# Kernel optimization log

Hardware: AMD Instinct MI355X
Metric: run time of the kernel (lower is better)

The kernel has to match this reference:

```python
import jax, jax.numpy as jnp
import numpy as np

GROUPS = 32
EPS = 1e-3  # keras GroupNormalization default epsilon

def group_norm(x, gamma, beta):
    B, H, W, C = x.shape
    g = GROUPS
    xg = x.reshape(B, H, W, g, C // g)
    mean = jnp.mean(xg, axis=(1, 2, 4), keepdims=True)
    var = jnp.var(xg, axis=(1, 2, 4), keepdims=True)
    xn = (xg - mean) * jax.lax.rsqrt(var + EPS)
    xn = xn.reshape(B, H, W, C)
    return xn * gamma + beta

def setup_inputs() -> dict:
    key = jax.random.key(0)
    ks = jax.random.split(key, 8)
    B, H, W, C = 16, 32, 32, 512
    s = C ** -0.5
    return {
        "x": jax.random.normal(ks[0], (B, H, W, C), jnp.float32),
        "gamma": jnp.ones((C,), jnp.float32),
        "beta": jnp.zeros((C,), jnp.float32),
        "wq": jax.random.normal(ks[1], (C, C), jnp.float32) * s,
        "bq": jnp.zeros((C,), jnp.float32),
        "wk": jax.random.normal(ks[2], (C, C), jnp.float32) * s,
        "bk": jnp.zeros((C,), jnp.float32),
        "wv": jax.random.normal(ks[3], (C, C), jnp.float32) * s,
        "bv": jnp.zeros((C,), jnp.float32),
        "wp": jax.random.normal(ks[4], (C, C), jnp.float32) * s,
        "bp": jnp.zeros((C,), jnp.float32),
        "index": 0,
    }

def reference(x, gamma, beta, wq, bq, wk, bk, wv, bv, wp, bp, index):
    B, H, W, C = x.shape
    N = H * W
    residual = x
    xn = group_norm(x, gamma, beta)
    xf = xn.reshape(B, N, C)
    q = xf @ wq + bq
    k = xf @ wk + bk
    v = xf @ wv + bv
    # full self-attention over all H*W positions (single head)
    scores = jnp.einsum('bnc,bmc->bnm', q, k) * (C ** -0.5)  # [B, N, N]
    attn = jax.nn.softmax(scores, axis=-1)
    out = jnp.einsum('bnm,bmc->bnc', attn, v)
    out = out @ wp + bp
    return out.reshape(B, H, W, C) + residual
```

## Files before the change

kernel.cpp:

```cpp
#include <hip/hip_runtime.h>

typedef __bf16 bf16;
typedef __bf16 bf16x8 __attribute__((ext_vector_type(8)));
typedef __bf16 bf16x4 __attribute__((ext_vector_type(4)));
typedef float  f32x4  __attribute__((ext_vector_type(4)));

#define CDIM   512
#define NPOS   1024
#define NBATCH 16
#define MTOT   (NBATCH * NPOS)
#define WELEMS (CDIM * CDIM)

#define OFF_WT  ((size_t)0)
#define OFF_XN  ((size_t)(2 * 1024 * 1024))
#define OFF_Q   (OFF_XN + (size_t)MTOT * CDIM * 2)
#define OFF_K   (OFF_Q  + (size_t)MTOT * CDIM * 2)
#define OFF_VT  (OFF_K  + (size_t)MTOT * CDIM * 2)
#define OFF_S   (OFF_VT + (size_t)MTOT * CDIM * 2)
#define OFF_P   (OFF_S  + (size_t)NBATCH * NPOS * NPOS * 4)
#define OFF_O   OFF_XN

__device__ __forceinline__ void gload16(const bf16* g, bf16* l) {
    __builtin_amdgcn_global_load_lds(
        (const __attribute__((address_space(1))) void*)g,
        (__attribute__((address_space(3))) void*)l, 16, 0, 0);
}

__global__ __launch_bounds__(256) void transpose_cast(
    const float* __restrict__ w0, const float* __restrict__ w1,
    const float* __restrict__ w2, const float* __restrict__ w3,
    bf16* __restrict__ wt)
{
    __shared__ bf16 tile[32][33];
    int z = blockIdx.z;
    const float* W = (z == 0) ? w0 : (z == 1) ? w1 : (z == 2) ? w2 : w3;
    bf16* out = wt + (size_t)z * WELEMS;
    int bx = blockIdx.x * 32;
    int by = blockIdx.y * 32;
    int tx = threadIdx.x & 31, ty = threadIdx.x >> 5;
    #pragma unroll
    for (int i = ty; i < 32; i += 8)
        tile[i][tx] = (bf16)W[(size_t)(by + i) * CDIM + bx + tx];
    __syncthreads();
    #pragma unroll
    for (int i = ty; i < 32; i += 8)
        out[(size_t)(bx + i) * CDIM + by + tx] = tile[tx][i];
}

__global__ __launch_bounds__(256) void groupnorm_kernel(
    const float* __restrict__ x, const float* __restrict__ gamma,
    const float* __restrict__ beta, bf16* __restrict__ xn)
{
    int b = blockIdx.x >> 5;
    int g = blockIdx.x & 31;
    const float* xb = x + (size_t)b * NPOS * CDIM;
    int t = threadIdx.x, lane = t & 63, wid = t >> 6;

    float s = 0.f, s2 = 0.f;
    for (int i = t; i < 4096; i += 256) {
        int n = i >> 2, c4 = i & 3;
        const float4 v = *(const float4*)&xb[n * CDIM + g * 16 + c4 * 4];
        s  += v.x + v.y + v.z + v.w;
        s2 += v.x * v.x + v.y * v.y + v.z * v.z + v.w * v.w;
    }
    #pragma unroll
    for (int o = 32; o; o >>= 1) { s += __shfl_xor(s, o); s2 += __shfl_xor(s2, o); }
    __shared__ float rs[4], rs2[4];
    if (lane == 0) { rs[wid] = s; rs2[wid] = s2; }
    __syncthreads();
    float S  = rs[0] + rs[1] + rs[2] + rs[3];
    float S2 = rs2[0] + rs2[1] + rs2[2] + rs2[3];
    const float inv_n = 1.f / 16384.f;
    float mean = S * inv_n;
    float var  = S2 * inv_n - mean * mean;
    float rstd = rsqrtf(var + 1e-3f);

    bf16* xnb = xn + (size_t)b * NPOS * CDIM;
    for (int i = t; i < 4096; i += 256) {
        int n = i >> 2, c4 = i & 3;
        int c = g * 16 + c4 * 4;
        const float4 v = *(const float4*)&xb[n * CDIM + c];
        bf16x4 o;
        o.x = (bf16)(((v.x - mean) * rstd) * gamma[c + 0] + beta[c + 0]);
        o.y = (bf16)(((v.y - mean) * rstd) * gamma[c + 1] + beta[c + 1]);
        o.z = (bf16)(((v.z - mean) * rstd) * gamma[c + 2] + beta[c + 2]);
        o.w = (bf16)(((v.w - mean) * rstd) * gamma[c + 3] + beta[c + 3]);
        *(bf16x4*)&xnb[n * CDIM + c] = o;
    }
}

#define BM 128
#define BN 128
#define BK 32

template<int MODE>
__global__ __launch_bounds__(256) void gemm_nt(
    const bf16* __restrict__ A, int lda, long strideA,
    const bf16* __restrict__ B, int ldb, long strideB,
    const float* __restrict__ bias, float scale,
    void* __restrict__ Cp, int ldc, long strideC,
    const float* __restrict__ resid, int K)
{
    __shared__ __align__(16) bf16 lsa[BM * BK];
    __shared__ __align__(16) bf16 lsb[BN * BK];
    const int z = blockIdx.z;
    A += (size_t)z * strideA;
    B += (size_t)z * strideB;
    const int bm = blockIdx.x * BM;
    const int bn = blockIdx.y * BN;
    const int t = threadIdx.x;
    const int lane = t & 63;
    const int wid = t >> 6;
    const int wr = (wid >> 1) * 64;
    const int wc = (wid & 1) * 64;
    const int lr = lane & 15;
    const int ks = lane >> 4;

    const int ci0 = t;
    const int r0 = ci0 >> 2, c0 = (ci0 & 3) * 8;
    const int ci1 = t + 256;
    const int r1 = ci1 >> 2, c1 = (ci1 & 3) * 8;

    f32x4 acc[4][4] = {};

    for (int k0 = 0; k0 < K; k0 += BK) {
        gload16(&A[(size_t)(bm + r0) * lda + k0 + c0], &lsa[ci0 * 8]);
        gload16(&A[(size_t)(bm + r1) * lda + k0 + c1], &lsa[ci1 * 8]);
        gload16(&B[(size_t)(bn + r0) * ldb + k0 + c0], &lsb[ci0 * 8]);
        gload16(&B[(size_t)(bn + r1) * ldb + k0 + c1], &lsb[ci1 * 8]);
        __syncthreads();
        bf16x8 af[4], bfr[4];
        #pragma unroll
        for (int m = 0; m < 4; m++)
            af[m] = *(const bf16x8*)&lsa[(wr + m * 16 + lr) * BK + ks * 8];
        #pragma unroll
        for (int n = 0; n < 4; n++)
            bfr[n] = *(const bf16x8*)&lsb[(wc + n * 16 + lr) * BK + ks * 8];
        #pragma unroll
        for (int m = 0; m < 4; m++)
            #pragma unroll
            for (int n = 0; n < 4; n++)
                acc[m][n] = __builtin_amdgcn_mfma_f32_16x16x32_bf16(af[m], bfr[n], acc[m][n], 0, 0, 0);
        __syncthreads();
    }

    #pragma unroll
    for (int m = 0; m < 4; m++) {
        #pragma unroll
        for (int n = 0; n < 4; n++) {
            const int row0 = bm + wr + m * 16 + ks * 4;
            const int col  = bn + wc + n * 16 + lr;
            const float bv = bias ? bias[col] : 0.f;
            #pragma unroll
            for (int r = 0; r < 4; r++) {
                const int rr = row0 + r;
                const float v = (acc[m][n][r] + bv) * scale;
                if (MODE == 0) {
                    ((bf16*)Cp)[(size_t)z * strideC + (size_t)rr * ldc + col] = (bf16)v;
                } else if (MODE == 1) {
                    const int bb = rr >> 10, nn = rr & 1023;
                    ((bf16*)Cp)[(size_t)bb * strideC + (size_t)col * ldc + nn] = (bf16)v;
                } else if (MODE == 2) {
                    ((float*)Cp)[(size_t)z * strideC + (size_t)rr * ldc + col] = v;
                } else {
                    const size_t idx = (size_t)rr * ldc + col;
                    ((float*)Cp)[idx] = v + resid[idx];
                }
            }
        }
    }
}

__global__ __launch_bounds__(256) void softmax_rows(
    const float* __restrict__ S, bf16* __restrict__ P)
{
    const size_t row = blockIdx.x;
    const float* s = S + row * NPOS;
    const int t = threadIdx.x, lane = t & 63, wid = t >> 6;
    float4 v = *(const float4*)&s[t * 4];

    float m = fmaxf(fmaxf(v.x, v.y), fmaxf(v.z, v.w));
    #pragma unroll
    for (int o = 32; o; o >>= 1) m = fmaxf(m, __shfl_xor(m, o));
    __shared__ float rmax[4], rsum[4];
    if (lane == 0) rmax[wid] = m;
    __syncthreads();
    m = fmaxf(fmaxf(rmax[0], rmax[1]), fmaxf(rmax[2], rmax[3]));

    float e0 = __expf(v.x - m), e1 = __expf(v.y - m);
    float e2 = __expf(v.z - m), e3 = __expf(v.w - m);
    float sum = e0 + e1 + e2 + e3;
    #pragma unroll
    for (int o = 32; o; o >>= 1) sum += __shfl_xor(sum, o);
    if (lane == 0) rsum[wid] = sum;
    __syncthreads();
    sum = rsum[0] + rsum[1] + rsum[2] + rsum[3];
    const float inv = 1.f / sum;

    bf16x4 o;
    o.x = (bf16)(e0 * inv); o.y = (bf16)(e1 * inv);
    o.z = (bf16)(e2 * inv); o.w = (bf16)(e3 * inv);
    *(bf16x4*)&P[row * NPOS + t * 4] = o;
}

extern "C" void kernel_launch(void* const* d_in, const int* in_sizes, int n_in,
                              void* d_out, int out_size, void* d_ws, size_t ws_size,
                              hipStream_t stream) {
    const float* x     = (const float*)d_in[0];
    const float* gamma = (const float*)d_in[1];
    const float* beta  = (const float*)d_in[2];
    const float* wq    = (const float*)d_in[3];
    const float* bq    = (const float*)d_in[4];
    const float* wk    = (const float*)d_in[5];
    const float* bk    = (const float*)d_in[6];
    const float* wv    = (const float*)d_in[7];
    const float* bv    = (const float*)d_in[8];
    const float* wp    = (const float*)d_in[9];
    const float* bp    = (const float*)d_in[10];

    char* ws = (char*)d_ws;
    bf16*  wt = (bf16*)(ws + OFF_WT);
    bf16*  xn = (bf16*)(ws + OFF_XN);
    bf16*  Q  = (bf16*)(ws + OFF_Q);
    bf16*  Km = (bf16*)(ws + OFF_K);
    bf16*  Vt = (bf16*)(ws + OFF_VT);
    float* Sc = (float*)(ws + OFF_S);
    bf16*  P  = (bf16*)(ws + OFF_P);
    bf16*  O  = (bf16*)(ws + OFF_O);

    transpose_cast<<<dim3(16, 16, 4), 256, 0, stream>>>(wq, wk, wv, wp, wt);
    groupnorm_kernel<<<dim3(512), 256, 0, stream>>>(x, gamma, beta, xn);

    const float qscale = 0.04419417382415922f;
    gemm_nt<0><<<dim3(128, 4, 1), 256, 0, stream>>>(
        xn, CDIM, 0, wt + 0 * WELEMS, CDIM, 0, bq, qscale, Q, CDIM, 0, nullptr, CDIM);
    gemm_nt<0><<<dim3(128, 4, 1), 256, 0, stream>>>(
        xn, CDIM, 0, wt + 1 * WELEMS, CDIM, 0, bk, 1.f, Km, CDIM, 0, nullptr, CDIM);
    gemm_nt<1><<<dim3(128, 4, 1), 256, 0, stream>>>(
        xn, CDIM, 0, wt + 2 * WELEMS, CDIM, 0, bv, 1.f, Vt, NPOS, (long)CDIM * NPOS, nullptr, CDIM);
    gemm_nt<2><<<dim3(8, 8, 16), 256, 0, stream>>>(
        Q, CDIM, (long)NPOS * CDIM, Km, CDIM, (long)NPOS * CDIM,
        nullptr, 1.f, Sc, NPOS, (long)NPOS * NPOS, nullptr, CDIM);
    softmax_rows<<<dim3(NBATCH * NPOS), 256, 0, stream>>>(Sc, P);
    gemm_nt<0><<<dim3(8, 4, 16), 256, 0, stream>>>(
        P, NPOS, (long)NPOS * NPOS, Vt, NPOS, (long)CDIM * NPOS,
        nullptr, 1.f, O, CDIM, (long)NPOS * CDIM, nullptr, NPOS);
    gemm_nt<3><<<dim3(128, 4, 1), 256, 0, stream>>>(
        O, CDIM, 0, wt + 3 * WELEMS, CDIM, 0, bp, 1.f, d_out, CDIM, 0, x, CDIM);
}
```

Baseline: 297.0 us.

## Fuse attention into flash kernel and merge QKV projections into one GEMM

Replaces the separate score GEMM, row softmax and PV GEMM with a single flash-attention kernel that keeps scores in registers and LDS, using online softmax with a lazy rescale threshold. This removes the 64MB fp32 score matrix and bf16 probability matrix round-trips through HBM. The three Q/K/V projection launches are merged into one GEMM grid keyed by region. The flash kernel launches only 256 blocks with one block per CU via launch bounds and large LDS, so occupancy and latency hiding may be limited.

```diff
diff --git a/kernel.cpp b/kernel.cpp
--- a/kernel.cpp
+++ b/kernel.cpp
@@ -16,14 +16,18 @@
 #define OFF_Q   (OFF_XN + (size_t)MTOT * CDIM * 2)
 #define OFF_K   (OFF_Q  + (size_t)MTOT * CDIM * 2)
 #define OFF_VT  (OFF_K  + (size_t)MTOT * CDIM * 2)
-#define OFF_S   (OFF_VT + (size_t)MTOT * CDIM * 2)
-#define OFF_P   (OFF_S  + (size_t)NBATCH * NPOS * NPOS * 4)
 #define OFF_O   OFF_XN
 
 __device__ __forceinline__ void gload16(const bf16* g, bf16* l) {
     __builtin_amdgcn_global_load_lds(
         (const __attribute__((address_space(1))) void*)g,
         (__attribute__((address_space(3))) void*)l, 16, 0, 0);
+}
+
+__device__ __forceinline__ unsigned int pk2(float lo, float hi) {
+    union { bf16 h; unsigned short s; } a, c;
+    a.h = (bf16)lo; c.h = (bf16)hi;
+    return (unsigned int)a.s | ((unsigned int)c.s << 16);
 }
 
 __global__ __launch_bounds__(256) void transpose_cast(
@@ -81,10 +85,10 @@
         int c = g * 16 + c4 * 4;
         const float4 v = *(const float4*)&xb[n * CDIM + c];
         bf16x4 o;
-        o.x = (bf16)(((v.x - mean) * rstd) * gamma[c + 0] + beta[c + 0]);
-        o.y = (bf16)(((v.y - mean) * rstd) * gamma[c + 1] + beta[c + 1]);
-        o.z = (bf16)(((v.z - mean) * rstd) * gamma[c + 2] + beta[c + 2]);
-        o.w = (bf16)(((v.w - mean) * rstd) * gamma[c + 3] + beta[c + 3]);
+        o[0] = (bf16)(((v.x - mean) * rstd) * gamma[c + 0] + beta[c + 0]);
+        o[1] = (bf16)(((v.y - mean) * rstd) * gamma[c + 1] + beta[c + 1]);
+        o[2] = (bf16)(((v.z - mean) * rstd) * gamma[c + 2] + beta[c + 2]);
+        o[3] = (bf16)(((v.w - mean) * rstd) * gamma[c + 3] + beta[c + 3]);
         *(bf16x4*)&xnb[n * CDIM + c] = o;
     }
 }
@@ -93,19 +97,229 @@
 #define BN 128
 #define BK 32
 
-template<int MODE>
-__global__ __launch_bounds__(256) void gemm_nt(
-    const bf16* __restrict__ A, int lda, long strideA,
-    const bf16* __restrict__ B, int ldb, long strideB,
-    const float* __restrict__ bias, float scale,
-    void* __restrict__ Cp, int ldc, long strideC,
-    const float* __restrict__ resid, int K)
+__global__ __launch_bounds__(256) void gemm_qkv(
+    const bf16* __restrict__ A, const bf16* __restrict__ Bw,
+    const float* __restrict__ bq, const float* __restrict__ bk,
+    const float* __restrict__ bv, float qscale,
+    bf16* __restrict__ Qo, bf16* __restrict__ Ko, bf16* __restrict__ Vto)
 {
     __shared__ __align__(16) bf16 lsa[BM * BK];
     __shared__ __align__(16) bf16 lsb[BN * BK];
-    const int z = blockIdx.z;
-    A += (size_t)z * strideA;
-    B += (size_t)z * strideB;
+    const int bm = blockIdx.x * BM;
+    const int bnG = blockIdx.y * BN;
+    const int region = blockIdx.y >> 2;
+    const int t = threadIdx.x;
+    const int lane = t & 63;
+    const int wid = t >> 6;
+    const int wr = (wid >> 1) * 64;
+    const int wc = (wid & 1) * 64;
+    const int lr = lane & 15;
+    const int ks = lane >> 4;
+
+    const int r0 = t >> 2, c0 = (t & 3) * 8;
+    const int r1 = (t + 256) >> 2, c1 = ((t + 256) & 3) * 8;
+
+    f32x4 acc[4][4] = {};
+
+    for (int k0 = 0; k0 < CDIM; k0 += BK) {
+        gload16(&A[(size_t)(bm + r0) * CDIM + k0 + c0], &lsa[t * 8]);
+        gload16(&A[(size_t)(bm + r1) * CDIM + k0 + c1], &lsa[(t + 256) * 8]);
+        gload16(&Bw[(size_t)(bnG + r0) * CDIM + k0 + c0], &lsb[t * 8]);
+        gload16(&Bw[(size_t)(bnG + r1) * CDIM + k0 + c1], &lsb[(t + 256) * 8]);
+        __syncthreads();
+        bf16x8 af[4], bfr[4];
+        #pragma unroll
+        for (int m = 0; m < 4; m++)
+            af[m] = *(const bf16x8*)&lsa[(wr + m * 16 + lr) * BK + ks * 8];
+        #pragma unroll
+        for (int n = 0; n < 4; n++)
+            bfr[n] = *(const bf16x8*)&lsb[(wc + n * 16 + lr) * BK + ks * 8];
+        #pragma unroll
+        for (int m = 0; m < 4; m++)
+            #pragma unroll
+            for (int n = 0; n < 4; n++)
+                acc[m][n] = __builtin_amdgcn_mfma_f32_16x16x32_bf16(af[m], bfr[n], acc[m][n], 0, 0, 0);
+        __syncthreads();
+    }
+
+    const float* bias = (region == 0) ? bq : (region == 1) ? bk : bv;
+    const float scale = (region == 0) ? qscale : 1.f;
+    #pragma unroll
+    for (int m = 0; m < 4; m++) {
+        #pragma unroll
+        for (int n = 0; n < 4; n++) {
+            const int row0 = bm + wr + m * 16 + ks * 4;
+            const int colG = bnG + wc + n * 16 + lr;
+            const int cl = colG - region * CDIM;
+            const float bvl = bias[cl];
+            #pragma unroll
+            for (int r = 0; r < 4; r++) {
+                const int rr = row0 + r;
+                const float v = (acc[m][n][r] + bvl) * scale;
+                if (region == 0) {
+                    Qo[(size_t)rr * CDIM + cl] = (bf16)v;
+                } else if (region == 1) {
+                    Ko[(size_t)rr * CDIM + cl] = (bf16)v;
+                } else {
+                    const int bb = rr >> 10, nn = rr & 1023;
+                    Vto[(size_t)bb * CDIM * NPOS + (size_t)cl * NPOS + nn] = (bf16)v;
+                }
+            }
+        }
+    }
+}
+
+#define QT 64
+#define KVB 64
+
+__global__ __launch_bounds__(256, 1) void flash_attn(
+    const bf16* __restrict__ Q, const bf16* __restrict__ K,
+    const bf16* __restrict__ Vt, bf16* __restrict__ O)
+{
+    __shared__ __align__(16) bf16 Klds[KVB * CDIM];
+    __shared__ __align__(16) bf16 Vlds[CDIM * KVB];
+    __shared__ unsigned int Plds[4][16 * 35];
+
+    const int p  = blockIdx.x;
+    const int b  = (p & 7) + 8 * ((p >> 3) >> 4);
+    const int qt = (p >> 3) & 15;
+
+    const int t = threadIdx.x;
+    const int lane = t & 63;
+    const int w = t >> 6;
+    const int lr = lane & 15;
+    const int g  = lane >> 4;
+
+    const bf16* Qg = Q  + ((size_t)b * NPOS + qt * QT) * CDIM;
+    const bf16* Kg = K  + (size_t)b * NPOS * CDIM;
+    const bf16* Vg = Vt + (size_t)b * CDIM * NPOS;
+
+    bf16x8 qf[16];
+    {
+        const bf16* qrow = Qg + (size_t)(w * 16 + lr) * CDIM + g * 8;
+        #pragma unroll
+        for (int ds = 0; ds < 16; ds++)
+            qf[ds] = *(const bf16x8*)(qrow + ds * 32);
+    }
+
+    f32x4 acc[32];
+    #pragma unroll
+    for (int i = 0; i < 32; i++) acc[i] = (f32x4){0.f, 0.f, 0.f, 0.f};
+    float m_run = -1e30f, l_run = 0.f;
+    unsigned int* Pw = Plds[w];
+
+    #pragma unroll
+    for (int i = 0; i < 16; i++) {
+        int ci = t + i * 256;
+        int r = ci >> 6, c = ci & 63;
+        gload16(Kg + (size_t)r * CDIM + ((c ^ (r & 7)) * 8), &Klds[ci * 8]);
+    }
+    __syncthreads();
+
+    for (int kt = 0; kt < 16; kt++) {
+        {
+            const int kv0 = kt * KVB;
+            #pragma unroll
+            for (int i = 0; i < 16; i++) {
+                int ci = t + i * 256;
+                int r = ci >> 3, c = ci & 7;
+                gload16(Vg + (size_t)r * NPOS + kv0 + ((c ^ (r & 7)) * 8), &Vlds[ci * 8]);
+            }
+        }
+        f32x4 s[4] = {};
+        #pragma unroll
+        for (int ds = 0; ds < 16; ds++) {
+            #pragma unroll
+            for (int k16 = 0; k16 < 4; k16++) {
+                const int row = k16 * 16 + lr;
+                const bf16x8 kf = *(const bf16x8*)&Klds[row * CDIM + (((ds * 4 + g) ^ (row & 7)) * 8)];
+                s[k16] = __builtin_amdgcn_mfma_f32_16x16x32_bf16(kf, qf[ds], s[k16], 0, 0, 0);
+            }
+        }
+        float mt = -1e30f;
+        #pragma unroll
+        for (int k16 = 0; k16 < 4; k16++)
+            #pragma unroll
+            for (int r = 0; r < 4; r++) mt = fmaxf(mt, s[k16][r]);
+        mt = fmaxf(mt, __shfl_xor(mt, 16));
+        mt = fmaxf(mt, __shfl_xor(mt, 32));
+        const float m_new = (mt > m_run + 8.f) ? mt : m_run;
+        float pr[16];
+        float ts = 0.f;
+        #pragma unroll
+        for (int k16 = 0; k16 < 4; k16++)
+            #pragma unroll
+            for (int r = 0; r < 4; r++) {
+                float e = __expf(s[k16][r] - m_new);
+                pr[k16 * 4 + r] = e; ts += e;
+            }
+        ts += __shfl_xor(ts, 16);
+        ts += __shfl_xor(ts, 32);
+        if (__any(m_new != m_run)) {
+            const float alpha = __expf(m_run - m_new);
+            #pragma unroll
+            for (int i = 0; i < 32; i++) {
+                acc[i][0] *= alpha; acc[i][1] *= alpha;
+                acc[i][2] *= alpha; acc[i][3] *= alpha;
+            }
+            l_run *= alpha;
+        }
+        l_run += ts;
+        m_run = m_new;
+        #pragma unroll
+        for (int k16 = 0; k16 < 4; k16++) {
+            Pw[lr * 35 + 8 * k16 + 2 * g + 0] = pk2(pr[k16 * 4 + 0], pr[k16 * 4 + 1]);
+            Pw[lr * 35 + 8 * k16 + 2 * g + 1] = pk2(pr[k16 * 4 + 2], pr[k16 * 4 + 3]);
+        }
+        __syncthreads();
+        if (kt < 15) {
+            const int kv0 = (kt + 1) * KVB;
+            #pragma unroll
+            for (int i = 0; i < 16; i++) {
+                int ci = t + i * 256;
+                int r = ci >> 6, c = ci & 63;
+                gload16(Kg + (size_t)(kv0 + r) * CDIM + ((c ^ (r & 7)) * 8), &Klds[ci * 8]);
+            }
+        }
+        bf16x8 pf[2];
+        #pragma unroll
+        for (int ks2 = 0; ks2 < 2; ks2++) {
+            union { unsigned int u[4]; bf16x8 v; } cvt;
+            #pragma unroll
+            for (int j = 0; j < 4; j++)
+                cvt.u[j] = Pw[lr * 35 + ks2 * 16 + g * 4 + j];
+            pf[ks2] = cvt.v;
+        }
+        #pragma unroll
+        for (int d16 = 0; d16 < 32; d16++) {
+            const int row = d16 * 16 + lr;
+            #pragma unroll
+            for (int ks2 = 0; ks2 < 2; ks2++) {
+                const bf16x8 vf = *(const bf16x8*)&Vlds[row * KVB + (((ks2 * 4 + g) ^ (row & 7)) * 8)];
+                acc[d16] = __builtin_amdgcn_mfma_f32_16x16x32_bf16(vf, pf[ks2], acc[d16], 0, 0, 0);
+            }
+        }
+        __syncthreads();
+    }
+
+    const float inv = 1.f / l_run;
+    bf16* Og = O + ((size_t)b * NPOS + qt * QT + w * 16 + lr) * CDIM;
+    #pragma unroll
+    for (int d16 = 0; d16 < 32; d16++) {
+        bf16x4 o;
+        o[0] = (bf16)(acc[d16][0] * inv); o[1] = (bf16)(acc[d16][1] * inv);
+        o[2] = (bf16)(acc[d16][2] * inv); o[3] = (bf16)(acc[d16][3] * inv);
+        *(bf16x4*)(Og + d16 * 16 + g * 4) = o;
+    }
+}
+
+__global__ __launch_bounds__(256) void gemm_proj(
+    const bf16* __restrict__ A, const bf16* __restrict__ Bw,
+    const float* __restrict__ bias, float* __restrict__ Cp,
+    const float* __restrict__ resid)
+{
+    __shared__ __align__(16) bf16 lsa[BM * BK];
+    __shared__ __align__(16) bf16 lsb[BN * BK];
     const int bm = blockIdx.x * BM;
     const int bn = blockIdx.y * BN;
     const int t = threadIdx.x;
@@ -115,19 +329,15 @@
     const int wc = (wid & 1) * 64;
     const int lr = lane & 15;
     const int ks = lane >> 4;
-
-    const int ci0 = t;
-    const int r0 = ci0 >> 2, c0 = (ci0 & 3) * 8;
-    const int ci1 = t + 256;
-    const int r1 = ci1 >> 2, c1 = (ci1 & 3) * 8;
+    const int r0 = t >> 2, c0 = (t & 3) * 8;
+    const int r1 = (t + 256) >> 2, c1 = ((t + 256) & 3) * 8;
 
     f32x4 acc[4][4] = {};
-
-    for (int k0 = 0; k0 < K; k0 += BK) {
-        gload16(&A[(size_t)(bm + r0) * lda + k0 + c0], &lsa[ci0 * 8]);
-        gload16(&A[(size_t)(bm + r1) * lda + k0 + c1], &lsa[ci1 * 8]);
-        gload16(&B[(size_t)(bn + r0) * ldb + k0 + c0], &lsb[ci0 * 8]);
-        gload16(&B[(size_t)(bn + r1) * ldb + k0 + c1], &lsb[ci1 * 8]);
+    for (int k0 = 0; k0 < CDIM; k0 += BK) {
+        gload16(&A[(size_t)(bm + r0) * CDIM + k0 + c0], &lsa[t * 8]);
+        gload16(&A[(size_t)(bm + r1) * CDIM + k0 + c1], &lsa[(t + 256) * 8]);
+        gload16(&Bw[(size_t)(bn + r0) * CDIM + k0 + c0], &lsb[t * 8]);
+        gload16(&Bw[(size_t)(bn + r1) * CDIM + k0 + c1], &lsb[(t + 256) * 8]);
         __syncthreads();
         bf16x8 af[4], bfr[4];
         #pragma unroll
@@ -143,64 +353,20 @@
                 acc[m][n] = __builtin_amdgcn_mfma_f32_16x16x32_bf16(af[m], bfr[n], acc[m][n], 0, 0, 0);
         __syncthreads();
     }
-
     #pragma unroll
     for (int m = 0; m < 4; m++) {
         #pragma unroll
         for (int n = 0; n < 4; n++) {
             const int row0 = bm + wr + m * 16 + ks * 4;
             const int col  = bn + wc + n * 16 + lr;
-            const float bv = bias ? bias[col] : 0.f;
+            const float bvl = bias[col];
             #pragma unroll
             for (int r = 0; r < 4; r++) {
-                const int rr = row0 + r;
-                const float v = (acc[m][n][r] + bv) * scale;
-                if (MODE == 0) {
-                    ((bf16*)Cp)[(size_t)z * strideC + (size_t)rr * ldc + col] = (bf16)v;
-                } else if (MODE == 1) {
-                    const int bb = rr >> 10, nn = rr & 1023;
-                    ((bf16*)Cp)[(size_t)bb * strideC + (size_t)col * ldc + nn] = (bf16)v;
-                } else if (MODE == 2) {
-                    ((float*)Cp)[(size_t)z * strideC + (size_t)rr * ldc + col] = v;
-                } else {
-                    const size_t idx = (size_t)rr * ldc + col;
-                    ((float*)Cp)[idx] = v + resid[idx];
-                }
-            }
-        }
-    }
-}
-
-__global__ __launch_bounds__(256) void softmax_rows(
-    const float* __restrict__ S, bf16* __restrict__ P)
-{
-    const size_t row = blockIdx.x;
-    const float* s = S + row * NPOS;
-    const int t = threadIdx.x, lane = t & 63, wid = t >> 6;
-    float4 v = *(const float4*)&s[t * 4];
-
-    float m = fmaxf(fmaxf(v.x, v.y), fmaxf(v.z, v.w));
-    #pragma unroll
-    for (int o = 32; o; o >>= 1) m = fmaxf(m, __shfl_xor(m, o));
-    __shared__ float rmax[4], rsum[4];
-    if (lane == 0) rmax[wid] = m;
-    __syncthreads();
-    m = fmaxf(fmaxf(rmax[0], rmax[1]), fmaxf(rmax[2], rmax[3]));
-
-    float e0 = __expf(v.x - m), e1 = __expf(v.y - m);
-    float e2 = __expf(v.z - m), e3 = __expf(v.w - m);
-    float sum = e0 + e1 + e2 + e3;
-    #pragma unroll
-    for (int o = 32; o; o >>= 1) sum += __shfl_xor(sum, o);
-    if (lane == 0) rsum[wid] = sum;
-    __syncthreads();
-    sum = rsum[0] + rsum[1] + rsum[2] + rsum[3];
-    const float inv = 1.f / sum;
-
-    bf16x4 o;
-    o.x = (bf16)(e0 * inv); o.y = (bf16)(e1 * inv);
-    o.z = (bf16)(e2 * inv); o.w = (bf16)(e3 * inv);
-    *(bf16x4*)&P[row * NPOS + t * 4] = o;
+                const size_t idx = (size_t)(row0 + r) * CDIM + col;
+                Cp[idx] = acc[m][n][r] + bvl + resid[idx];
+            }
+        }
+    }
 }
 
 extern "C" void kernel_launch(void* const* d_in, const int* in_sizes, int n_in,
@@ -219,32 +385,22 @@
     const float* bp    = (const float*)d_in[10];
 
     char* ws = (char*)d_ws;
-    bf16*  wt = (bf16*)(ws + OFF_WT);
-    bf16*  xn = (bf16*)(ws + OFF_XN);
-    bf16*  Q  = (bf16*)(ws + OFF_Q);
-    bf16*  Km = (bf16*)(ws + OFF_K);
-    bf16*  Vt = (bf16*)(ws + OFF_VT);
-    float* Sc = (float*)(ws + OFF_S);
-    bf16*  P  = (bf16*)(ws + OFF_P);
-    bf16*  O  = (bf16*)(ws + OFF_O);
+    bf16* wt = (bf16*)(ws + OFF_WT);
+    bf16* xn = (bf16*)(ws + OFF_XN);
+    bf16* Q  = (bf16*)(ws + OFF_Q);
+    bf16* Km = (bf16*)(ws + OFF_K);
+    bf16* Vt = (bf16*)(ws + OFF_VT);
+    bf16* O  = (bf16*)(ws + OFF_O);
 
     transpose_cast<<<dim3(16, 16, 4), 256, 0, stream>>>(wq, wk, wv, wp, wt);
     groupnorm_kernel<<<dim3(512), 256, 0, stream>>>(x, gamma, beta, xn);
 
     const float qscale = 0.04419417382415922f;
-    gemm_nt<0><<<dim3(128, 4, 1), 256, 0, stream>>>(
-        xn, CDIM, 0, wt + 0 * WELEMS, CDIM, 0, bq, qscale, Q, CDIM, 0, nullptr, CDIM);
-    gemm_nt<0><<<dim3(128, 4, 1), 256, 0, stream>>>(
-        xn, CDIM, 0, wt + 1 * WELEMS, CDIM, 0, bk, 1.f, Km, CDIM, 0, nullptr, CDIM);
-    gemm_nt<1><<<dim3(128, 4, 1), 256, 0, stream>>>(
-        xn, CDIM, 0, wt + 2 * WELEMS, CDIM, 0, bv, 1.f, Vt, NPOS, (long)CDIM * NPOS, nullptr, CDIM);
-    gemm_nt<2><<<dim3(8, 8, 16), 256, 0, stream>>>(
-        Q, CDIM, (long)NPOS * CDIM, Km, CDIM, (long)NPOS * CDIM,
-        nullptr, 1.f, Sc, NPOS, (long)NPOS * NPOS, nullptr, CDIM);
-    softmax_rows<<<dim3(NBATCH * NPOS), 256, 0, stream>>>(Sc, P);
-    gemm_nt<0><<<dim3(8, 4, 16), 256, 0, stream>>>(
-        P, NPOS, (long)NPOS * NPOS, Vt, NPOS, (long)CDIM * NPOS,
-        nullptr, 1.f, O, CDIM, (long)NPOS * CDIM, nullptr, NPOS);
-    gemm_nt<3><<<dim3(128, 4, 1), 256, 0, stream>>>(
-        O, CDIM, 0, wt + 3 * WELEMS, CDIM, 0, bp, 1.f, d_out, CDIM, 0, x, CDIM);
-}
+    gemm_qkv<<<dim3(128, 12), 256, 0, stream>>>(
+        xn, wt, bq, bk, bv, qscale, Q, Km, Vt);
+
+    flash_attn<<<dim3(256), 256, 0, stream>>>(Q, Km, Vt, O);
+
+    gemm_proj<<<dim3(128, 4), 256, 0, stream>>>(
+        O, wt + (size_t)3 * WELEMS, bp, (float*)d_out, x);
+}
```

Result: faster. 261.3 us (-12.0%).
